# Optimization experiments

Measured on AMD Instinct MI355X. Metric: run time of the kernel, lower is better.

Reference implementation:

```python
import jax, jax.numpy as jnp
import numpy as np

B, DIM, COND, HID = 500000, 3, 64, 128
IN = DIM + COND + 1  # z + context + time feature


def setup_inputs() -> dict:
    key = jax.random.key(0)
    ks = jax.random.split(key, 8)
    s_in = 1.0 / np.sqrt(IN)
    s_h = 1.0 / np.sqrt(HID)
    return {
        "t": jnp.float32(0.5),
        "z": jax.random.normal(ks[0], (B, DIM), jnp.float32),
        "logp": jnp.zeros((B, 1), jnp.float32),
        "context": jax.random.normal(ks[1], (B, COND), jnp.float32),
        "eps": jax.random.normal(ks[2], (B, DIM), jnp.float32),
        "W_in": jax.random.normal(ks[3], (IN, HID), jnp.float32) * s_in,
        "b_in": jnp.zeros((HID,), jnp.float32),
        "W_h1": jax.random.normal(ks[4], (HID, HID), jnp.float32) * s_h,
        "b_h1": jnp.zeros((HID,), jnp.float32),
        "W_h2": jax.random.normal(ks[5], (HID, HID), jnp.float32) * s_h,
        "b_h2": jnp.zeros((HID,), jnp.float32),
        "W_out": jax.random.normal(ks[6], (HID, DIM), jnp.float32) * s_h,
        "b_out": jnp.zeros((DIM,), jnp.float32),
        "out_scale": jnp.float32(1.0),
    }


def reference(t, z, logp, context, eps, W_in, b_in, W_h1, b_h1, W_h2, b_h2,
              W_out, b_out, out_scale):
    t_feat = jnp.full((z.shape[0], 1), t, dtype=z.dtype)

    def vel(zz):
        inp = jnp.concatenate([zz, context, t_feat], axis=1)  # (B, IN)
        h = jnp.tanh(inp @ W_in + b_in)
        h = jnp.tanh(h @ W_h1 + b_h1)
        h = jnp.tanh(h @ W_h2 + b_h2)
        return (h @ W_out + b_out) * out_scale  # (B, DIM)

    # Hutchinson trace: tr(df/dz) ~= eps^T (d/dz)(f . eps) via vjp with cotangent eps
    f, vjp_fn = jax.vjp(vel, z)
    (gz,) = vjp_fn(eps)
    neg_div = -jnp.sum(gz * eps, axis=1, keepdims=True)  # (B, 1)
    return f, neg_div
```

## Files before the change

### kernel.cpp

```cpp
#include <hip/hip_runtime.h>


#define B_N    500000
#define NT32   15625
#define GRID   256
#define WPB    8
#define NSTR   (GRID * WPB)

#define L_WFIN   0
#define L_WF1    8704
#define L_WF2    25600
#define L_WB2    42496
#define L_WB1    59392
#define L_WOUTP  76288
#define L_WOUTT  76800
#define L_WIN3   77196
#define L_F16END 77592
#define N_BIAS   384
#define PREP_N   (L_F16END + N_BIAS)
#define BIAS_BYTE   155184
#define OUTST_BYTE  156720
#define LDS_BYTES   159792
#define COPY16      9795

typedef _Float16 f16x4 __attribute__((ext_vector_type(4)));
typedef _Float16 f16x8 __attribute__((ext_vector_type(8)));
typedef float    f32x4 __attribute__((ext_vector_type(4)));

static __device__ inline f16x4 lds_a4(const _Float16* p) {
    return *reinterpret_cast<const f16x4*>(p);
}
static __device__ inline f16x8 lds_a8(const _Float16* p) {
    f16x4 lo = *reinterpret_cast<const f16x4*>(p);
    f16x4 hi = *reinterpret_cast<const f16x4*>(p + 4);
    return __builtin_shufflevector(lo, hi, 0, 1, 2, 3, 4, 5, 6, 7);
}

#define MFMA16(a, b, c) __builtin_amdgcn_mfma_f32_16x16x16f16((a), (b), (c), 0, 0, 0)
#define MFMA32(a, b, c) __builtin_amdgcn_mfma_f32_16x16x32_f16((a), (b), (c), 0, 0, 0)

static __device__ inline float ftanh(float x) {
    float e = __expf(2.f * x);
    return 1.f - 2.f * __builtin_amdgcn_rcpf(e + 1.f);
}

#define TANH4(dst, sub, acv, bb)                               \
    dst[(sub) * 4 + 0] = (_Float16)ftanh((acv)[0] + (bb).x);   \
    dst[(sub) * 4 + 1] = (_Float16)ftanh((acv)[1] + (bb).y);   \
    dst[(sub) * 4 + 2] = (_Float16)ftanh((acv)[2] + (bb).z);   \
    dst[(sub) * 4 + 3] = (_Float16)ftanh((acv)[3] + (bb).w);

static __device__ inline int sig(int p) {
    return (p & ~31) | ((p & 4) << 2) | ((p >> 1) & 12) | (p & 3);
}

__global__ void prep_kernel(const float* __restrict__ W_in,
                            const float* __restrict__ W_h1,
                            const float* __restrict__ W_h2,
                            const float* __restrict__ W_out,
                            const float* __restrict__ b_in,
                            const float* __restrict__ b_h1,
                            const float* __restrict__ b_h2,
                            _Float16* __restrict__ ws) {
    int i = blockIdx.x * 256 + threadIdx.x;
    if (i >= PREP_N) return;
    if (i >= L_F16END) {
        int bi = i - L_F16END;
        float* bp = reinterpret_cast<float*>(ws + L_F16END);
        bp[bi] = (bi < 128) ? b_in[bi] : (bi < 256) ? b_h1[bi - 128]
                                                    : b_h2[bi - 256];
        return;
    }
    float v = 0.f;
    if (i < L_WF1) {
        int n = i / 68, k = i - n * 68;
        if      (k < 64)  v = W_in[(3 + k) * 128 + n];
        else if (k < 67)  v = W_in[(k - 64) * 128 + n];
        else              v = W_in[67 * 128 + n];
    } else if (i < L_WF2) {
        int j = i - L_WF1; int n = j / 132, a = j - n * 132;
        if (a < 128) v = W_h1[sig(a) * 128 + n];
    } else if (i < L_WB2) {
        int j = i - L_WF2; int n = j / 132, a = j - n * 132;
        if (a < 128) v = W_h2[sig(a) * 128 + n];
    } else if (i < L_WB1) {
        int j = i - L_WB2; int r = j / 132, b = j - r * 132;
        if (b < 128) v = W_h2[r * 128 + sig(b)];
    } else if (i < L_WOUTP) {
        int j = i - L_WB1; int r = j / 132, b = j - r * 132;
        if (b < 128) v = W_h1[r * 128 + sig(b)];
    } else if (i < L_WOUTT) {
        int j = i - L_WOUTP; int n = j >> 2, k = j & 3;
        if (k < 3) v = W_out[n * 3 + k];
    } else if (i < L_WIN3) {
        int j = i - L_WOUTT; int d = j / 132, n = j - d * 132;
        if (n < 128) v = W_out[sig(n) * 3 + d];
    } else {
        int j = i - L_WIN3; int d = j / 132, a = j - d * 132;
        if (a < 128) v = W_in[d * 128 + sig(a)];
    }
    ws[i] = (_Float16)v;
}

__global__ __launch_bounds__(512, 1) void fused_kernel(
        const float* __restrict__ t_p,  const float* __restrict__ z,
        const float* __restrict__ ctx,  const float* __restrict__ eps,
        const float* __restrict__ b_out, const float* __restrict__ os_p,
        const _Float16* __restrict__ ws, float* __restrict__ out) {
    extern __shared__ _Float16 smem[];
    const int tid  = threadIdx.x;
    const int wave = tid >> 6;
    const int lane = tid & 63;
    const int l15  = lane & 15;
    const int q    = lane >> 4;

    {
        const uint4* src = reinterpret_cast<const uint4*>(ws);
        uint4* dst = reinterpret_cast<uint4*>(smem);
        for (int i = tid; i < COPY16; i += 512) dst[i] = src[i];
    }
    __syncthreads();

    const _Float16* WFIN  = smem + L_WFIN;
    const _Float16* WF1   = smem + L_WF1;
    const _Float16* WF2   = smem + L_WF2;
    const _Float16* WB2   = smem + L_WB2;
    const _Float16* WB1   = smem + L_WB1;
    const _Float16* WOUTP = smem + L_WOUTP;
    const _Float16* WOUTT = smem + L_WOUTT;
    const _Float16* WIN3  = smem + L_WIN3;
    const float* biasf =
        reinterpret_cast<const float*>(reinterpret_cast<char*>(smem) + BIAS_BYTE);
    float* outst =
        reinterpret_cast<float*>(reinterpret_cast<char*>(smem) + OUTST_BYTE)
        + wave * 96;

    const float tval = t_p[0];
    const float os   = os_p[0];
    const float bo0 = b_out[0], bo1 = b_out[1], bo2 = b_out[2];
    float* out_f  = out;
    float* out_nd = out + (size_t)B_N * 3;

    const f32x4 zero4 = {0.f, 0.f, 0.f, 0.f};
    const _Float16 hz = (_Float16)0.f;

    for (int t = blockIdx.x * WPB + wave; t < NT32; t += NSTR) {
        const int gb = t * 32;

        f16x4 epsb[2];
        float ee[2][3];
        #pragma unroll
        for (int c = 0; c < 2; ++c) {
            f16x4 ev = {hz, hz, hz, hz};
            ee[c][0] = ee[c][1] = ee[c][2] = 0.f;
            if (q == 0) {
                const float* ep = eps + (size_t)(gb + 16 * c + l15) * 3;
                ee[c][0] = ep[0]; ee[c][1] = ep[1]; ee[c][2] = ep[2];
                ev[0] = (_Float16)ee[c][0];
                ev[1] = (_Float16)ee[c][1];
                ev[2] = (_Float16)ee[c][2];
            }
            epsb[c] = ev;
        }

        f16x8 cb[2][2];
        #pragma unroll
        for (int a = 0; a < 2; ++a)
            #pragma unroll
            for (int c = 0; c < 2; ++c) {
                const float* cp = ctx + (size_t)(gb + 16 * c + l15) * 64
                                  + a * 32 + 8 * q;
                const float4 v0 = *reinterpret_cast<const float4*>(cp);
                const float4 v1 = *reinterpret_cast<const float4*>(cp + 4);
                f16x8 cv;
                cv[0] = (_Float16)v0.x; cv[1] = (_Float16)v0.y;
                cv[2] = (_Float16)v0.z; cv[3] = (_Float16)v0.w;
                cv[4] = (_Float16)v1.x; cv[5] = (_Float16)v1.y;
                cv[6] = (_Float16)v1.z; cv[7] = (_Float16)v1.w;
                cb[a][c] = cv;
            }
        f16x4 bz[2];
        #pragma unroll
        for (int c = 0; c < 2; ++c) {
            f16x4 zv = {hz, hz, hz, hz};
            if (q == 0) {
                const float* zp = z + (size_t)(gb + 16 * c + l15) * 3;
                zv[0] = (_Float16)zp[0]; zv[1] = (_Float16)zp[1];
                zv[2] = (_Float16)zp[2]; zv[3] = (_Float16)tval;
            }
            bz[c] = zv;
        }

        f16x8 h1p[4][2];
        #pragma unroll
        for (int m = 0; m < 8; ++m) {
            f32x4 a0 = zero4, a1 = zero4;
            #pragma unroll
            for (int a = 0; a < 2; ++a) {
                f16x8 A = lds_a8(WFIN + (16 * m + l15) * 68 + a * 32 + 8 * q);
                a0 = MFMA32(A, cb[a][0], a0);
                a1 = MFMA32(A, cb[a][1], a1);
            }
            {
                f16x4 A4 = lds_a4(WFIN + (16 * m + l15) * 68 + 64 + 4 * q);
                a0 = MFMA16(A4, bz[0], a0);
                a1 = MFMA16(A4, bz[1], a1);
            }
            const float4 bb = *reinterpret_cast<const float4*>(
                biasf + 0 + 16 * m + 4 * q);
            TANH4(h1p[m >> 1][0], m & 1, a0, bb);
            TANH4(h1p[m >> 1][1], m & 1, a1, bb);
        }

        f16x8 h2p[4][2];
        #pragma unroll
        for (int m = 0; m < 8; ++m) {
            f32x4 a0 = zero4, a1 = zero4;
            #pragma unroll
            for (int a = 0; a < 4; ++a) {
                f16x8 A = lds_a8(WF1 + (16 * m + l15) * 132 + a * 32 + 8 * q);
                a0 = MFMA32(A, h1p[a][0], a0);
                a1 = MFMA32(A, h1p[a][1], a1);
            }
            const float4 bb = *reinterpret_cast<const float4*>(
                biasf + 128 + 16 * m + 4 * q);
            TANH4(h2p[m >> 1][0], m & 1, a0, bb);
            TANH4(h2p[m >> 1][1], m & 1, a1, bb);
        }

        f16x8 u3p[4][2];
        f32x4 f0 = zero4, f1 = zero4;
        #pragma unroll
        for (int mp = 0; mp < 4; ++mp) {
            f16x8 h3p0, h3p1;
            #pragma unroll
            for (int sub = 0; sub < 2; ++sub) {
                const int m = 2 * mp + sub;
                f32x4 a0 = zero4, a1 = zero4;
                #pragma unroll
                for (int a = 0; a < 4; ++a) {
                    f16x8 A = lds_a8(WF2 + (16 * m + l15) * 132 + a * 32 + 8 * q);
                    a0 = MFMA32(A, h2p[a][0], a0);
                    a1 = MFMA32(A, h2p[a][1], a1);
                }
                f16x4 a3 = lds_a4(WOUTP + (16 * m + l15) * 4 + 4 * q);
                f32x4 up0 = MFMA16(a3, epsb[0], zero4);
                f32x4 up1 = MFMA16(a3, epsb[1], zero4);
                const float4 bb = *reinterpret_cast<const float4*>(
                    biasf + 256 + 16 * m + 4 * q);
                #pragma unroll
                for (int i = 0; i < 4; ++i) {
                    float bi = (i == 0) ? bb.x : (i == 1) ? bb.y
                              : (i == 2) ? bb.z : bb.w;
                    float h0 = ftanh(a0[i] + bi);
                    float h1v = ftanh(a1[i] + bi);
                    h3p0[sub * 4 + i] = (_Float16)h0;
                    h3p1[sub * 4 + i] = (_Float16)h1v;
                    u3p[mp][0][sub * 4 + i] =
                        (_Float16)(os * up0[i] * (1.f - h0 * h0));
                    u3p[mp][1][sub * 4 + i] =
                        (_Float16)(os * up1[i] * (1.f - h1v * h1v));
                }
            }
            f16x8 Af = lds_a8(WOUTT + l15 * 132 + mp * 32 + 8 * q);
            f0 = MFMA32(Af, h3p0, f0);
            f1 = MFMA32(Af, h3p1, f1);
        }
        if (q == 0) {
            outst[(0 * 16 + l15) * 3 + 0] = (f0[0] + bo0) * os;
            outst[(0 * 16 + l15) * 3 + 1] = (f0[1] + bo1) * os;
            outst[(0 * 16 + l15) * 3 + 2] = (f0[2] + bo2) * os;
            outst[(1 * 16 + l15) * 3 + 0] = (f1[0] + bo0) * os;
            outst[(1 * 16 + l15) * 3 + 1] = (f1[1] + bo1) * os;
            outst[(1 * 16 + l15) * 3 + 2] = (f1[2] + bo2) * os;
        }

        #pragma unroll
        for (int m = 0; m < 8; ++m) {
            f32x4 a0 = zero4, a1 = zero4;
            #pragma unroll
            for (int a = 0; a < 4; ++a) {
                f16x8 A = lds_a8(WB2 + (16 * m + l15) * 132 + a * 32 + 8 * q);
                a0 = MFMA32(A, u3p[a][0], a0);
                a1 = MFMA32(A, u3p[a][1], a1);
            }
            #pragma unroll
            for (int i = 0; i < 4; ++i) {
                float h0 = (float)h2p[m >> 1][0][(m & 1) * 4 + i];
                float h1v = (float)h2p[m >> 1][1][(m & 1) * 4 + i];
                h2p[m >> 1][0][(m & 1) * 4 + i] =
                    (_Float16)(a0[i] * (1.f - h0 * h0));
                h2p[m >> 1][1][(m & 1) * 4 + i] =
                    (_Float16)(a1[i] * (1.f - h1v * h1v));
            }
        }

        f32x4 g0 = zero4, g1 = zero4;
        #pragma unroll
        for (int mp = 0; mp < 4; ++mp) {
            f16x8 u1p0, u1p1;
            #pragma unroll
            for (int sub = 0; sub < 2; ++sub) {
                const int m = 2 * mp + sub;
                f32x4 a0 = zero4, a1 = zero4;
                #pragma unroll
                for (int a = 0; a < 4; ++a) {
                    f16x8 A = lds_a8(WB1 + (16 * m + l15) * 132 + a * 32 + 8 * q);
                    a0 = MFMA32(A, h2p[a][0], a0);
                    a1 = MFMA32(A, h2p[a][1], a1);
                }
                #pragma unroll
                for (int i = 0; i < 4; ++i) {
                    float h0 = (float)h1p[mp][0][sub * 4 + i];
                    float h1v = (float)h1p[mp][1][sub * 4 + i];
                    u1p0[sub * 4 + i] = (_Float16)(a0[i] * (1.f - h0 * h0));
                    u1p1[sub * 4 + i] = (_Float16)(a1[i] * (1.f - h1v * h1v));
                }
            }
            f16x8 Ag = lds_a8(WIN3 + l15 * 132 + mp * 32 + 8 * q);
            g0 = MFMA32(Ag, u1p0, g0);
            g1 = MFMA32(Ag, u1p1, g1);
        }
        if (q == 0) {
            out_nd[gb + l15] =
                -(g0[0] * ee[0][0] + g0[1] * ee[0][1] + g0[2] * ee[0][2]);
            out_nd[gb + 16 + l15] =
                -(g1[0] * ee[1][0] + g1[1] * ee[1][1] + g1[2] * ee[1][2]);
        }

        if (lane < 24) {
            float4 v = *reinterpret_cast<const float4*>(outst + lane * 4);
            *reinterpret_cast<float4*>(out_f + (size_t)gb * 3 + lane * 4) = v;
        }
    }
}

extern "C" void kernel_launch(void* const* d_in, const int* in_sizes, int n_in,
                              void* d_out, int out_size, void* d_ws, size_t ws_size,
                              hipStream_t stream) {
    const float* t_p   = (const float*)d_in[0];
    const float* z     = (const float*)d_in[1];
    const float* ctx   = (const float*)d_in[3];
    const float* eps   = (const float*)d_in[4];
    const float* W_in  = (const float*)d_in[5];
    const float* b_in  = (const float*)d_in[6];
    const float* W_h1  = (const float*)d_in[7];
    const float* b_h1  = (const float*)d_in[8];
    const float* W_h2  = (const float*)d_in[9];
    const float* b_h2  = (const float*)d_in[10];
    const float* W_out = (const float*)d_in[11];
    const float* b_out = (const float*)d_in[12];
    const float* os_p  = (const float*)d_in[13];
    _Float16* ws = (_Float16*)d_ws;
    float* out = (float*)d_out;

    static bool attr_set = false;
    if (!attr_set) {
        (void)hipFuncSetAttribute((const void*)fused_kernel,
                                  hipFuncAttributeMaxDynamicSharedMemorySize,
                                  LDS_BYTES);
        attr_set = true;
    }

    prep_kernel<<<(PREP_N + 255) / 256, 256, 0, stream>>>(
        W_in, W_h1, W_h2, W_out, b_in, b_h1, b_h2, ws);
    fused_kernel<<<GRID, 512, LDS_BYTES, stream>>>(
        t_p, z, ctx, eps, b_out, os_p, ws, out);
}
```

Measured before the change: 310.4 us.

## Pad LDS weight rows to 136, use packed f16 converts and packed backward math

Weight rows in LDS are padded from 132 to 136 halves so each A-fragment is fetched with a single 16-byte load instead of two 8-byte loads. Float-to-half conversions now use packed round-toward-zero converts, and the backward tanh-derivative products run in packed f16 arithmetic instead of f32. The output scale is folded into eps up front, and the LDS staging of the f output is replaced by direct scalar global stores. This cuts VALU and LDS instruction count but lowers precision (RTZ rounding, f16 derivative math) and makes the f stores less coalesced.

Result: slower. 1.115 ms (+259.3%).

```diff
diff --git a/kernel.cpp b/kernel.cpp
--- a/kernel.cpp
+++ b/kernel.cpp
@@ -9,20 +9,21 @@
 
 #define L_WFIN   0
 #define L_WF1    8704
-#define L_WF2    25600
-#define L_WB2    42496
-#define L_WB1    59392
-#define L_WOUTP  76288
-#define L_WOUTT  76800
-#define L_WIN3   77196
-#define L_F16END 77592
+#define L_WF2    26112
+#define L_WB2    43520
+#define L_WB1    60928
+#define L_WOUTP  78336
+#define L_WOUTT  78848
+#define L_WIN3   79256
+#define L_F16END 79664
 #define N_BIAS   384
 #define PREP_N   (L_F16END + N_BIAS)
-#define BIAS_BYTE   155184
-#define OUTST_BYTE  156720
-#define LDS_BYTES   159792
-#define COPY16      9795
-
+#define BIAS_BYTE   159328
+#define COPY_BYTES  160864
+#define COPY16      10054
+#define LDS_BYTES   162848
+
+typedef _Float16 f16x2 __attribute__((ext_vector_type(2)));
 typedef _Float16 f16x4 __attribute__((ext_vector_type(4)));
 typedef _Float16 f16x8 __attribute__((ext_vector_type(8)));
 typedef float    f32x4 __attribute__((ext_vector_type(4)));
@@ -35,20 +36,22 @@
     f16x4 hi = *reinterpret_cast<const f16x4*>(p + 4);
     return __builtin_shufflevector(lo, hi, 0, 1, 2, 3, 4, 5, 6, 7);
 }
+static __device__ inline f16x8 lds_a8x(const _Float16* p) {
+    return *reinterpret_cast<const f16x8*>(p);
+}
 
 #define MFMA16(a, b, c) __builtin_amdgcn_mfma_f32_16x16x16f16((a), (b), (c), 0, 0, 0)
 #define MFMA32(a, b, c) __builtin_amdgcn_mfma_f32_16x16x32_f16((a), (b), (c), 0, 0, 0)
+
+static __device__ inline f16x2 pkrtz(float x, float y) {
+    auto r = __builtin_amdgcn_cvt_pkrtz(x, y);
+    return __builtin_bit_cast(f16x2, r);
+}
 
 static __device__ inline float ftanh(float x) {
     float e = __expf(2.f * x);
     return 1.f - 2.f * __builtin_amdgcn_rcpf(e + 1.f);
 }
-
-#define TANH4(dst, sub, acv, bb)                               \
-    dst[(sub) * 4 + 0] = (_Float16)ftanh((acv)[0] + (bb).x);   \
-    dst[(sub) * 4 + 1] = (_Float16)ftanh((acv)[1] + (bb).y);   \
-    dst[(sub) * 4 + 2] = (_Float16)ftanh((acv)[2] + (bb).z);   \
-    dst[(sub) * 4 + 3] = (_Float16)ftanh((acv)[3] + (bb).w);
 
 static __device__ inline int sig(int p) {
     return (p & ~31) | ((p & 4) << 2) | ((p >> 1) & 12) | (p & 3);
@@ -78,25 +81,25 @@
         else if (k < 67)  v = W_in[(k - 64) * 128 + n];
         else              v = W_in[67 * 128 + n];
     } else if (i < L_WF2) {
-        int j = i - L_WF1; int n = j / 132, a = j - n * 132;
+        int j = i - L_WF1; int n = j / 136, a = j - n * 136;
         if (a < 128) v = W_h1[sig(a) * 128 + n];
     } else if (i < L_WB2) {
-        int j = i - L_WF2; int n = j / 132, a = j - n * 132;
+        int j = i - L_WF2; int n = j / 136, a = j - n * 136;
         if (a < 128) v = W_h2[sig(a) * 128 + n];
     } else if (i < L_WB1) {
-        int j = i - L_WB2; int r = j / 132, b = j - r * 132;
+        int j = i - L_WB2; int r = j / 136, b = j - r * 136;
         if (b < 128) v = W_h2[r * 128 + sig(b)];
     } else if (i < L_WOUTP) {
-        int j = i - L_WB1; int r = j / 132, b = j - r * 132;
+        int j = i - L_WB1; int r = j / 136, b = j - r * 136;
         if (b < 128) v = W_h1[r * 128 + sig(b)];
     } else if (i < L_WOUTT) {
         int j = i - L_WOUTP; int n = j >> 2, k = j & 3;
         if (k < 3) v = W_out[n * 3 + k];
     } else if (i < L_WIN3) {
-        int j = i - L_WOUTT; int d = j / 132, n = j - d * 132;
+        int j = i - L_WOUTT; int d = j / 136, n = j - d * 136;
         if (n < 128) v = W_out[sig(n) * 3 + d];
     } else {
-        int j = i - L_WIN3; int d = j / 132, a = j - d * 132;
+        int j = i - L_WIN3; int d = j / 136, a = j - d * 136;
         if (a < 128) v = W_in[d * 128 + sig(a)];
     }
     ws[i] = (_Float16)v;
@@ -131,9 +134,6 @@
     const _Float16* WIN3  = smem + L_WIN3;
     const float* biasf =
         reinterpret_cast<const float*>(reinterpret_cast<char*>(smem) + BIAS_BYTE);
-    float* outst =
-        reinterpret_cast<float*>(reinterpret_cast<char*>(smem) + OUTST_BYTE)
-        + wave * 96;
 
     const float tval = t_p[0];
     const float os   = os_p[0];
@@ -143,6 +143,7 @@
 
     const f32x4 zero4 = {0.f, 0.f, 0.f, 0.f};
     const _Float16 hz = (_Float16)0.f;
+    const f16x2 one2 = {(_Float16)1.f, (_Float16)1.f};
 
     for (int t = blockIdx.x * WPB + wave; t < NT32; t += NSTR) {
         const int gb = t * 32;
@@ -156,9 +157,9 @@
             if (q == 0) {
                 const float* ep = eps + (size_t)(gb + 16 * c + l15) * 3;
                 ee[c][0] = ep[0]; ee[c][1] = ep[1]; ee[c][2] = ep[2];
-                ev[0] = (_Float16)ee[c][0];
-                ev[1] = (_Float16)ee[c][1];
-                ev[2] = (_Float16)ee[c][2];
+                f16x2 p01 = pkrtz(ee[c][0] * os, ee[c][1] * os);
+                f16x2 p23 = pkrtz(ee[c][2] * os, 0.f);
+                ev[0] = p01[0]; ev[1] = p01[1]; ev[2] = p23[0];
             }
             epsb[c] = ev;
         }
@@ -173,10 +174,10 @@
                 const float4 v0 = *reinterpret_cast<const float4*>(cp);
                 const float4 v1 = *reinterpret_cast<const float4*>(cp + 4);
                 f16x8 cv;
-                cv[0] = (_Float16)v0.x; cv[1] = (_Float16)v0.y;
-                cv[2] = (_Float16)v0.z; cv[3] = (_Float16)v0.w;
-                cv[4] = (_Float16)v1.x; cv[5] = (_Float16)v1.y;
-                cv[6] = (_Float16)v1.z; cv[7] = (_Float16)v1.w;
+                f16x2 p0 = pkrtz(v0.x, v0.y), p1 = pkrtz(v0.z, v0.w);
+                f16x2 p2 = pkrtz(v1.x, v1.y), p3 = pkrtz(v1.z, v1.w);
+                cv[0] = p0[0]; cv[1] = p0[1]; cv[2] = p1[0]; cv[3] = p1[1];
+                cv[4] = p2[0]; cv[5] = p2[1]; cv[6] = p3[0]; cv[7] = p3[1];
                 cb[a][c] = cv;
             }
         f16x4 bz[2];
@@ -185,8 +186,9 @@
             f16x4 zv = {hz, hz, hz, hz};
             if (q == 0) {
                 const float* zp = z + (size_t)(gb + 16 * c + l15) * 3;
-                zv[0] = (_Float16)zp[0]; zv[1] = (_Float16)zp[1];
-                zv[2] = (_Float16)zp[2]; zv[3] = (_Float16)tval;
+                f16x2 p01 = pkrtz(zp[0], zp[1]);
+                f16x2 p23 = pkrtz(zp[2], tval);
+                zv[0] = p01[0]; zv[1] = p01[1]; zv[2] = p23[0]; zv[3] = p23[1];
             }
             bz[c] = zv;
         }
@@ -208,8 +210,15 @@
             }
             const float4 bb = *reinterpret_cast<const float4*>(
                 biasf + 0 + 16 * m + 4 * q);
-            TANH4(h1p[m >> 1][0], m & 1, a0, bb);
-            TANH4(h1p[m >> 1][1], m & 1, a1, bb);
+            f16x2 h0a = pkrtz(ftanh(a0[0] + bb.x), ftanh(a0[1] + bb.y));
+            f16x2 h0b = pkrtz(ftanh(a0[2] + bb.z), ftanh(a0[3] + bb.w));
+            f16x2 h1a = pkrtz(ftanh(a1[0] + bb.x), ftanh(a1[1] + bb.y));
+            f16x2 h1b = pkrtz(ftanh(a1[2] + bb.z), ftanh(a1[3] + bb.w));
+            const int s4 = (m & 1) * 4;
+            h1p[m >> 1][0][s4 + 0] = h0a[0]; h1p[m >> 1][0][s4 + 1] = h0a[1];
+            h1p[m >> 1][0][s4 + 2] = h0b[0]; h1p[m >> 1][0][s4 + 3] = h0b[1];
+            h1p[m >> 1][1][s4 + 0] = h1a[0]; h1p[m >> 1][1][s4 + 1] = h1a[1];
+            h1p[m >> 1][1][s4 + 2] = h1b[0]; h1p[m >> 1][1][s4 + 3] = h1b[1];
         }
 
         f16x8 h2p[4][2];
@@ -218,14 +227,21 @@
             f32x4 a0 = zero4, a1 = zero4;
             #pragma unroll
             for (int a = 0; a < 4; ++a) {
-                f16x8 A = lds_a8(WF1 + (16 * m + l15) * 132 + a * 32 + 8 * q);
+                f16x8 A = lds_a8x(WF1 + (16 * m + l15) * 136 + a * 32 + 8 * q);
                 a0 = MFMA32(A, h1p[a][0], a0);
                 a1 = MFMA32(A, h1p[a][1], a1);
             }
             const float4 bb = *reinterpret_cast<const float4*>(
                 biasf + 128 + 16 * m + 4 * q);
-            TANH4(h2p[m >> 1][0], m & 1, a0, bb);
-            TANH4(h2p[m >> 1][1], m & 1, a1, bb);
+            f16x2 h0a = pkrtz(ftanh(a0[0] + bb.x), ftanh(a0[1] + bb.y));
+            f16x2 h0b = pkrtz(ftanh(a0[2] + bb.z), ftanh(a0[3] + bb.w));
+            f16x2 h1a = pkrtz(ftanh(a1[0] + bb.x), ftanh(a1[1] + bb.y));
+            f16x2 h1b = pkrtz(ftanh(a1[2] + bb.z), ftanh(a1[3] + bb.w));
+            const int s4 = (m & 1) * 4;
+            h2p[m >> 1][0][s4 + 0] = h0a[0]; h2p[m >> 1][0][s4 + 1] = h0a[1];
+            h2p[m >> 1][0][s4 + 2] = h0b[0]; h2p[m >> 1][0][s4 + 3] = h0b[1];
+            h2p[m >> 1][1][s4 + 0] = h1a[0]; h2p[m >> 1][1][s4 + 1] = h1a[1];
+            h2p[m >> 1][1][s4 + 2] = h1b[0]; h2p[m >> 1][1][s4 + 3] = h1b[1];
         }
 
         f16x8 u3p[4][2];
@@ -239,7 +255,7 @@
                 f32x4 a0 = zero4, a1 = zero4;
                 #pragma unroll
                 for (int a = 0; a < 4; ++a) {
-                    f16x8 A = lds_a8(WF2 + (16 * m + l15) * 132 + a * 32 + 8 * q);
+                    f16x8 A = lds_a8x(WF2 + (16 * m + l15) * 136 + a * 32 + 8 * q);
                     a0 = MFMA32(A, h2p[a][0], a0);
                     a1 = MFMA32(A, h2p[a][1], a1);
                 }
@@ -248,31 +264,43 @@
                 f32x4 up1 = MFMA16(a3, epsb[1], zero4);
                 const float4 bb = *reinterpret_cast<const float4*>(
                     biasf + 256 + 16 * m + 4 * q);
-                #pragma unroll
-                for (int i = 0; i < 4; ++i) {
-                    float bi = (i == 0) ? bb.x : (i == 1) ? bb.y
-                              : (i == 2) ? bb.z : bb.w;
-                    float h0 = ftanh(a0[i] + bi);
-                    float h1v = ftanh(a1[i] + bi);
-                    h3p0[sub * 4 + i] = (_Float16)h0;
-                    h3p1[sub * 4 + i] = (_Float16)h1v;
-                    u3p[mp][0][sub * 4 + i] =
-                        (_Float16)(os * up0[i] * (1.f - h0 * h0));
-                    u3p[mp][1][sub * 4 + i] =
-                        (_Float16)(os * up1[i] * (1.f - h1v * h1v));
-                }
-            }
-            f16x8 Af = lds_a8(WOUTT + l15 * 132 + mp * 32 + 8 * q);
+                float t0 = ftanh(a0[0] + bb.x), t1 = ftanh(a0[1] + bb.y);
+                float t2 = ftanh(a0[2] + bb.z), t3 = ftanh(a0[3] + bb.w);
+                f16x2 hp0 = pkrtz(t0, t1), hp1 = pkrtz(t2, t3);
+                f16x2 up01 = pkrtz(up0[0] * __builtin_fmaf(-t0, t0, 1.f),
+                                   up0[1] * __builtin_fmaf(-t1, t1, 1.f));
+                f16x2 up23 = pkrtz(up0[2] * __builtin_fmaf(-t2, t2, 1.f),
+                                   up0[3] * __builtin_fmaf(-t3, t3, 1.f));
+                float s0 = ftanh(a1[0] + bb.x), s1 = ftanh(a1[1] + bb.y);
+                float s2 = ftanh(a1[2] + bb.z), s3 = ftanh(a1[3] + bb.w);
+                f16x2 hq0 = pkrtz(s0, s1), hq1 = pkrtz(s2, s3);
+                f16x2 uq01 = pkrtz(up1[0] * __builtin_fmaf(-s0, s0, 1.f),
+                                   up1[1] * __builtin_fmaf(-s1, s1, 1.f));
+                f16x2 uq23 = pkrtz(up1[2] * __builtin_fmaf(-s2, s2, 1.f),
+                                   up1[3] * __builtin_fmaf(-s3, s3, 1.f));
+                const int s4 = sub * 4;
+                h3p0[s4 + 0] = hp0[0]; h3p0[s4 + 1] = hp0[1];
+                h3p0[s4 + 2] = hp1[0]; h3p0[s4 + 3] = hp1[1];
+                h3p1[s4 + 0] = hq0[0]; h3p1[s4 + 1] = hq0[1];
+                h3p1[s4 + 2] = hq1[0]; h3p1[s4 + 3] = hq1[1];
+                u3p[mp][0][s4 + 0] = up01[0]; u3p[mp][0][s4 + 1] = up01[1];
+                u3p[mp][0][s4 + 2] = up23[0]; u3p[mp][0][s4 + 3] = up23[1];
+                u3p[mp][1][s4 + 0] = uq01[0]; u3p[mp][1][s4 + 1] = uq01[1];
+                u3p[mp][1][s4 + 2] = uq23[0]; u3p[mp][1][s4 + 3] = uq23[1];
+            }
+            f16x8 Af = lds_a8x(WOUTT + l15 * 136 + mp * 32 + 8 * q);
             f0 = MFMA32(Af, h3p0, f0);
             f1 = MFMA32(Af, h3p1, f1);
         }
         if (q == 0) {
-            outst[(0 * 16 + l15) * 3 + 0] = (f0[0] + bo0) * os;
-            outst[(0 * 16 + l15) * 3 + 1] = (f0[1] + bo1) * os;
-            outst[(0 * 16 + l15) * 3 + 2] = (f0[2] + bo2) * os;
-            outst[(1 * 16 + l15) * 3 + 0] = (f1[0] + bo0) * os;
-            outst[(1 * 16 + l15) * 3 + 1] = (f1[1] + bo1) * os;
-            outst[(1 * 16 + l15) * 3 + 2] = (f1[2] + bo2) * os;
+            const size_t r0 = (size_t)(gb + l15) * 3;
+            out_f[r0 + 0] = (f0[0] + bo0) * os;
+            out_f[r0 + 1] = (f0[1] + bo1) * os;
+            out_f[r0 + 2] = (f0[2] + bo2) * os;
+            const size_t r1 = (size_t)(gb + 16 + l15) * 3;
+            out_f[r1 + 0] = (f1[0] + bo0) * os;
+            out_f[r1 + 1] = (f1[1] + bo1) * os;
+            out_f[r1 + 2] = (f1[2] + bo2) * os;
         }
 
         #pragma unroll
@@ -280,18 +308,28 @@
             f32x4 a0 = zero4, a1 = zero4;
             #pragma unroll
             for (int a = 0; a < 4; ++a) {
-                f16x8 A = lds_a8(WB2 + (16 * m + l15) * 132 + a * 32 + 8 * q);
+                f16x8 A = lds_a8x(WB2 + (16 * m + l15) * 136 + a * 32 + 8 * q);
                 a0 = MFMA32(A, u3p[a][0], a0);
                 a1 = MFMA32(A, u3p[a][1], a1);
             }
-            #pragma unroll
-            for (int i = 0; i < 4; ++i) {
-                float h0 = (float)h2p[m >> 1][0][(m & 1) * 4 + i];
-                float h1v = (float)h2p[m >> 1][1][(m & 1) * 4 + i];
-                h2p[m >> 1][0][(m & 1) * 4 + i] =
-                    (_Float16)(a0[i] * (1.f - h0 * h0));
-                h2p[m >> 1][1][(m & 1) * 4 + i] =
-                    (_Float16)(a1[i] * (1.f - h1v * h1v));
+            const int s4 = (m & 1) * 4;
+            {
+                f16x2 aa01 = pkrtz(a0[0], a0[1]), aa23 = pkrtz(a0[2], a0[3]);
+                f16x2 h01 = {h2p[m >> 1][0][s4 + 0], h2p[m >> 1][0][s4 + 1]};
+                f16x2 h23 = {h2p[m >> 1][0][s4 + 2], h2p[m >> 1][0][s4 + 3]};
+                f16x2 u01 = aa01 * (one2 - h01 * h01);
+                f16x2 u23 = aa23 * (one2 - h23 * h23);
+                h2p[m >> 1][0][s4 + 0] = u01[0]; h2p[m >> 1][0][s4 + 1] = u01[1];
+                h2p[m >> 1][0][s4 + 2] = u23[0]; h2p[m >> 1][0][s4 + 3] = u23[1];
+            }
+            {
+                f16x2 aa01 = pkrtz(a1[0], a1[1]), aa23 = pkrtz(a1[2], a1[3]);
+                f16x2 h01 = {h2p[m >> 1][1][s4 + 0], h2p[m >> 1][1][s4 + 1]};
+                f16x2 h23 = {h2p[m >> 1][1][s4 + 2], h2p[m >> 1][1][s4 + 3]};
+                f16x2 u01 = aa01 * (one2 - h01 * h01);
+                f16x2 u23 = aa23 * (one2 - h23 * h23);
+                h2p[m >> 1][1][s4 + 0] = u01[0]; h2p[m >> 1][1][s4 + 1] = u01[1];
+                h2p[m >> 1][1][s4 + 2] = u23[0]; h2p[m >> 1][1][s4 + 3] = u23[1];
             }
         }
 
@@ -305,19 +343,31 @@
                 f32x4 a0 = zero4, a1 = zero4;
                 #pragma unroll
                 for (int a = 0; a < 4; ++a) {
-                    f16x8 A = lds_a8(WB1 + (16 * m + l15) * 132 + a * 32 + 8 * q);
+                    f16x8 A = lds_a8x(WB1 + (16 * m + l15) * 136 + a * 32 + 8 * q);
                     a0 = MFMA32(A, h2p[a][0], a0);
                     a1 = MFMA32(A, h2p[a][1], a1);
                 }
-                #pragma unroll
-                for (int i = 0; i < 4; ++i) {
-                    float h0 = (float)h1p[mp][0][sub * 4 + i];
-                    float h1v = (float)h1p[mp][1][sub * 4 + i];
-                    u1p0[sub * 4 + i] = (_Float16)(a0[i] * (1.f - h0 * h0));
-                    u1p1[sub * 4 + i] = (_Float16)(a1[i] * (1.f - h1v * h1v));
+                const int s4 = sub * 4;
+                {
+                    f16x2 aa01 = pkrtz(a0[0], a0[1]), aa23 = pkrtz(a0[2], a0[3]);
+                    f16x2 h01 = {h1p[mp][0][s4 + 0], h1p[mp][0][s4 + 1]};
+                    f16x2 h23 = {h1p[mp][0][s4 + 2], h1p[mp][0][s4 + 3]};
+                    f16x2 u01 = aa01 * (one2 - h01 * h01);
+                    f16x2 u23 = aa23 * (one2 - h23 * h23);
+                    u1p0[s4 + 0] = u01[0]; u1p0[s4 + 1] = u01[1];
+                    u1p0[s4 + 2] = u23[0]; u1p0[s4 + 3] = u23[1];
                 }
-            }
-            f16x8 Ag = lds_a8(WIN3 + l15 * 132 + mp * 32 + 8 * q);
+                {
+                    f16x2 aa01 = pkrtz(a1[0], a1[1]), aa23 = pkrtz(a1[2], a1[3]);
+                    f16x2 h01 = {h1p[mp][1][s4 + 0], h1p[mp][1][s4 + 1]};
+                    f16x2 h23 = {h1p[mp][1][s4 + 2], h1p[mp][1][s4 + 3]};
+                    f16x2 u01 = aa01 * (one2 - h01 * h01);
+                    f16x2 u23 = aa23 * (one2 - h23 * h23);
+                    u1p1[s4 + 0] = u01[0]; u1p1[s4 + 1] = u01[1];
+                    u1p1[s4 + 2] = u23[0]; u1p1[s4 + 3] = u23[1];
+                }
+            }
+            f16x8 Ag = lds_a8x(WIN3 + l15 * 136 + mp * 32 + 8 * q);
             g0 = MFMA32(Ag, u1p0, g0);
             g1 = MFMA32(Ag, u1p1, g1);
         }
@@ -326,11 +376,6 @@
                 -(g0[0] * ee[0][0] + g0[1] * ee[0][1] + g0[2] * ee[0][2]);
             out_nd[gb + 16 + l15] =
                 -(g1[0] * ee[1][0] + g1[1] * ee[1][1] + g1[2] * ee[1][2]);
-        }
-
-        if (lane < 24) {
-            float4 v = *reinterpret_cast<const float4*>(outst + lane * 4);
-            *reinterpret_cast<float4*>(out_f + (size_t)gb * 3 + lane * 4) = v;
         }
     }
 }
```
